# Kernel optimization log

Hardware: AMD Instinct MI355X
Metric: run time of the kernel (lower is better)

Reference implementation:

```python
import jax, jax.numpy as jnp
import numpy as np

N_NODES = 100000
N_EDGES = 1600000
EMBED = 64
HEADS = 8
HEAD_DIM = EMBED // HEADS
FFN = 4 * EMBED
EPS = 1e-5


def _layer_norm(x, g, b):
    m = jnp.mean(x, axis=-1, keepdims=True)
    v = jnp.mean(jnp.square(x - m), axis=-1, keepdims=True)
    return (x - m) * jax.lax.rsqrt(v + EPS) * g + b


def setup_inputs() -> dict:
    key = jax.random.key(0)
    ks = jax.random.split(key, 10)
    s = lambda fan_in: 1.0 / np.sqrt(fan_in)
    x = jax.random.normal(ks[0], (N_NODES, EMBED), dtype=jnp.float32)
    edge_indices = jax.random.randint(ks[1], (2, N_EDGES), 0, N_NODES, dtype=jnp.int64)
    attn_w = jax.random.uniform(ks[2], (EMBED, 3 * EMBED), jnp.float32, -s(EMBED), s(EMBED))
    attn_b = jnp.zeros((3 * EMBED,), jnp.float32)
    w1 = jax.random.uniform(ks[3], (EMBED, FFN), jnp.float32, -s(EMBED), s(EMBED))
    b1 = jnp.zeros((FFN,), jnp.float32)
    w2 = jax.random.uniform(ks[4], (FFN, EMBED), jnp.float32, -s(FFN), s(FFN))
    b2 = jnp.zeros((EMBED,), jnp.float32)
    ln1_g = jnp.ones((EMBED,), jnp.float32)
    ln1_b = jnp.zeros((EMBED,), jnp.float32)
    ln2_g = jnp.ones((EMBED,), jnp.float32)
    ln2_b = jnp.zeros((EMBED,), jnp.float32)
    return {"x": x, "edge_indices": edge_indices, "attn_w": attn_w, "attn_b": attn_b,
            "w1": w1, "b1": b1, "w2": w2, "b2": b2,
            "ln1_g": ln1_g, "ln1_b": ln1_b, "ln2_g": ln2_g, "ln2_b": ln2_b}


def _self_attention(x, edge_indices, attn_w, attn_b):
    n = x.shape[0]
    row, col = edge_indices[0], edge_indices[1]
    scale = EMBED ** (-0.5)  # note: original scales by embed_dim**-0.5
    qkv = (x @ attn_w + attn_b).reshape(n, HEADS, 3 * HEAD_DIM)
    q, k, v = jnp.split(qkv, 3, axis=2)  # each [N, H, Dh]
    alpha = jnp.sum(q[row] * k[col], axis=2) * scale  # [E, H]
    # sparse per-row softmax via segment reductions
    m = jax.ops.segment_max(alpha, row, num_segments=n)  # [N, H]
    e = jnp.exp(alpha - m[row])
    denom = jax.ops.segment_sum(e, row, num_segments=n)  # [N, H]
    weights = e / denom[row]  # [E, H]
    vals = v[col] * weights[:, :, None]  # [E, H, Dh]
    out = jax.ops.segment_sum(vals, row, num_segments=n)  # [N, H, Dh]
    return out.reshape(n, EMBED)


def reference(x, edge_indices, attn_w, attn_b, w1, b1, w2, b2, ln1_g, ln1_b, ln2_g, ln2_b):
    # post-norm (norm_first=False), dropout=0
    x = _layer_norm(x + _self_attention(x, edge_indices, attn_w, attn_b), ln1_g, ln1_b)
    ffn = jax.nn.relu(x @ w1 + b1) @ w2 + b2
    x = _layer_norm(x + ffn, ln2_g, ln2_b)
    return x
```

## Files before the change

kernel.cpp:

```cpp
#include <hip/hip_runtime.h>
#include <hip/hip_bf16.h>
#include <hip/hip_fp8.h>


#define WAVE 64
constexpr int BUCKET_SHIFT = 7;
constexpr int NBMAX = 800;

typedef __attribute__((ext_vector_type(8))) short bf16x8;
typedef __attribute__((ext_vector_type(4))) float f32x4;
typedef __attribute__((ext_vector_type(2))) float f32x2;

union BF8 {
  bf16x8 v;
  unsigned u[4];
};

__device__ __forceinline__ float bfbits_lo(unsigned u) {
  return __uint_as_float(u << 16);
}
__device__ __forceinline__ float bfbits_hi(unsigned u) {
  return __uint_as_float(u & 0xffff0000u);
}
__device__ __forceinline__ unsigned f2bf_pk(float a, float b) {
  unsigned ua = __float_as_uint(a);
  unsigned ub = __float_as_uint(b);
  ua = (ua + 0x7fff + ((ua >> 16) & 1)) >> 16;
  ub = (ub + 0x7fff + ((ub >> 16) & 1)) & 0xffff0000u;
  return ua | ub;
}
__device__ __forceinline__ unsigned short f2bf1(float a) {
  unsigned ua = __float_as_uint(a);
  ua = (ua + 0x7fff + ((ua >> 16) & 1)) >> 16;
  return (unsigned short)ua;
}

#if defined(__has_builtin)
#if __has_builtin(__builtin_amdgcn_cvt_pk_f32_fp8) && \
    __has_builtin(__builtin_amdgcn_cvt_pk_fp8_f32)
#define FP8_HW 1
#endif
#endif

#ifdef FP8_HW
#define FP8PK0(w) __builtin_amdgcn_cvt_pk_f32_fp8((int)(w), false)
#define FP8PK1(w) __builtin_amdgcn_cvt_pk_f32_fp8((int)(w), true)
__device__ __forceinline__ unsigned fp8enc4(float a, float b, float c,
                                            float d) {
  int r = __builtin_amdgcn_cvt_pk_fp8_f32(a, b, 0, false);
  r = __builtin_amdgcn_cvt_pk_fp8_f32(c, d, r, true);
  return (unsigned)r;
}
#else
__device__ __forceinline__ f32x2 fp8pk_sw(unsigned w, int sh) {
  __hip_fp8_e4m3 a, b;
  a.__x = (unsigned char)((w >> sh) & 0xff);
  b.__x = (unsigned char)((w >> (sh + 8)) & 0xff);
  f32x2 r;
  r.x = (float)a;
  r.y = (float)b;
  return r;
}
#define FP8PK0(w) fp8pk_sw((w), 0)
#define FP8PK1(w) fp8pk_sw((w), 16)
__device__ __forceinline__ unsigned fp8enc4(float a, float b, float c,
                                            float d) {
  __hip_fp8_e4m3 qa(a), qb(b), qc(c), qd(d);
  return (unsigned)qa.__x | ((unsigned)qb.__x << 8) |
         ((unsigned)qc.__x << 16) | ((unsigned)qd.__x << 24);
}
#endif

__device__ __forceinline__ float dot8_fp8(uint2 w, const float qv[8]) {
  f32x2 a = FP8PK0(w.x), b = FP8PK1(w.x), c = FP8PK0(w.y), d = FP8PK1(w.y);
  return a.x * qv[0] + a.y * qv[1] + b.x * qv[2] + b.y * qv[3] + c.x * qv[4] +
         c.y * qv[5] + d.x * qv[6] + d.y * qv[7];
}
__device__ __forceinline__ void acc8_fp8(uint2 w, float ee, float acc[8]) {
  f32x2 a = FP8PK0(w.x), b = FP8PK1(w.x), c = FP8PK0(w.y), d = FP8PK1(w.y);
  acc[0] += ee * a.x;
  acc[1] += ee * a.y;
  acc[2] += ee * b.x;
  acc[3] += ee * b.y;
  acc[4] += ee * c.x;
  acc[5] += ee * c.y;
  acc[6] += ee * d.x;
  acc[7] += ee * d.y;
}

__device__ __forceinline__ bool detect_is64_block(const int* __restrict__ e,
                                                  int* sflag) {
  if (threadIdx.x == 0) *sflag = 0;
  __syncthreads();
  unsigned v = 0;
  for (int i = threadIdx.x; i < 2048; i += blockDim.x)
    v |= (unsigned)e[2 * i + 1];
  if (v) atomicOr(sflag, 1);
  __syncthreads();
  return *sflag == 0;
}

__device__ __forceinline__ int edge_row(const int* e, int i, bool is64) {
  return is64 ? e[2 * (size_t)i] : e[i];
}
__device__ __forceinline__ int edge_col(const int* e, int i, int E, bool is64) {
  return is64 ? e[2 * ((size_t)E + i)] : e[(size_t)E + i];
}

__global__ __launch_bounds__(256) void cvt_w2(
    const float* __restrict__ aw, const float* __restrict__ w1,
    const float* __restrict__ w2, unsigned short* __restrict__ awT,
    unsigned short* __restrict__ w1T, unsigned short* __restrict__ w2T) {
  int tid = blockIdx.x * 256 + threadIdx.x;
  int stride = gridDim.x * 256;
  for (int i = tid; i < 192 * 64; i += stride) {
    int nn = i >> 6, kk = i & 63;
    awT[i] = f2bf1(aw[kk * 192 + nn]);
  }
  for (int i = tid; i < 256 * 64; i += stride) {
    int nn = i >> 6, kk = i & 63;
    w1T[i] = f2bf1(w1[kk * 256 + nn]);
  }
  for (int i = tid; i < 64 * 256; i += stride) {
    int nn = i >> 8, kk = i & 255;
    w2T[i] = f2bf1(w2[kk * 64 + nn]);
  }
}

__global__ __launch_bounds__(256) void bucket_count(const int* __restrict__ e,
                                                    int E,
                                                    int* __restrict__ tot,
                                                    int NB, int CH) {
  __shared__ int h[NBMAX];
  __shared__ int sflag;
  bool is64 = detect_is64_block(e, &sflag);
  for (int b = threadIdx.x; b < NB; b += 256) h[b] = 0;
  __syncthreads();
  int c0 = blockIdx.x * CH, c1 = min(E, c0 + CH);
  for (int i = c0 + threadIdx.x; i < c1; i += 256)
    atomicAdd(&h[edge_row(e, i, is64) >> BUCKET_SHIFT], 1);
  __syncthreads();
  for (int b = threadIdx.x; b < NB; b += 256)
    if (h[b]) atomicAdd(&tot[b], h[b]);
}

__global__ __launch_bounds__(1024) void scan_buckets(
    const int* __restrict__ tot, int NB, int* __restrict__ bucketstart,
    int* __restrict__ cursor) {
  __shared__ int wtot[16], wexcl[16];
  int tid = threadIdx.x;
  int lane = tid & 63, wid = tid >> 6;
  int v = (tid < NB) ? tot[tid] : 0;
  int incl = v;
#pragma unroll
  for (int m = 1; m < WAVE; m <<= 1) {
    int t = __shfl_up(incl, m);
    if (lane >= m) incl += t;
  }
  if (lane == 63) wtot[wid] = incl;
  __syncthreads();
  if (tid < 16) {
    int w = wtot[tid];
    int wi = w;
#pragma unroll
    for (int m = 1; m < 16; m <<= 1) {
      int t = __shfl_up(wi, m);
      if (tid >= m) wi += t;
    }
    wexcl[tid] = wi - w;
  }
  __syncthreads();
  int excl = wexcl[wid] + incl - v;
  if (tid < NB) {
    bucketstart[tid] = excl;
    cursor[tid] = excl;
  }
  if (tid == NB - 1) bucketstart[NB] = excl + v;
}

__global__ __launch_bounds__(256) void bucket_place(const int* __restrict__ e,
                                                    int E,
                                                    int* __restrict__ cursor,
                                                    unsigned* __restrict__ ebuf,
                                                    int NB, int CH) {
  __shared__ int cnt[NBMAX];
  __shared__ int sflag;
  bool is64 = detect_is64_block(e, &sflag);
  for (int b = threadIdx.x; b < NB; b += 256) cnt[b] = 0;
  __syncthreads();
  int c0 = blockIdx.x * CH, c1 = min(E, c0 + CH);
  for (int i = c0 + threadIdx.x; i < c1; i += 256)
    atomicAdd(&cnt[edge_row(e, i, is64) >> BUCKET_SHIFT], 1);
  __syncthreads();
  for (int b = threadIdx.x; b < NB; b += 256) {
    int c = cnt[b];
    cnt[b] = c ? atomicAdd(&cursor[b], c) : 0;
  }
  __syncthreads();
  for (int i = c0 + threadIdx.x; i < c1; i += 256) {
    int r = edge_row(e, i, is64);
    int c = edge_col(e, i, E, is64);
    int pos = atomicAdd(&cnt[r >> BUCKET_SHIFT], 1);
    ebuf[pos] = ((unsigned)(r & 127) << 17) | (unsigned)c;
  }
}

__global__ __launch_bounds__(256) void bucket_csr(
    const unsigned* __restrict__ ebuf, const int* __restrict__ bucketstart,
    int* __restrict__ ecol, int* __restrict__ rowstart, int n, int NB, int E) {
  __shared__ int cnt[128], offs[128], cur[128];
  const int b = blockIdx.x;
  const int tid = threadIdx.x;
  const int start = bucketstart[b];
  const int end = bucketstart[b + 1];
  if (tid < 128) cnt[tid] = 0;
  __syncthreads();
  for (int i = start + tid; i < end; i += 256)
    atomicAdd(&cnt[(ebuf[i] >> 17) & 127], 1);
  __syncthreads();
  if (tid < 128) offs[tid] = cnt[tid];
  __syncthreads();
  for (int s = 1; s < 128; s <<= 1) {
    int t = 0;
    if (tid < 128 && tid >= s) t = offs[tid - s];
    __syncthreads();
    if (tid < 128) offs[tid] += t;
    __syncthreads();
  }
  if (tid < 128) {
    int excl = offs[tid] - cnt[tid];
    cur[tid] = start + excl;
    int gr = (b << BUCKET_SHIFT) + tid;
    if (gr < n) rowstart[gr] = start + excl;
  }
  if (b == NB - 1 && tid == 0) rowstart[n] = E;
  __syncthreads();
  for (int i = start + tid; i < end; i += 256) {
    unsigned p = ebuf[i];
    int pos = atomicAdd(&cur[(p >> 17) & 127], 1);
    ecol[pos] = (int)(p & 0x1FFFF);
  }
}

template <int NCOLS, int K, int MODE, bool AFP32>
__global__ __launch_bounds__(256) void mfma_gemm(
    const void* __restrict__ A, const unsigned short* __restrict__ BT,
    const float* __restrict__ bias, unsigned short* __restrict__ out_q,
    unsigned char* __restrict__ out_kv8, unsigned short* __restrict__ out_h,
    const unsigned short* __restrict__ resid, const float* __restrict__ g,
    const float* __restrict__ beta, float* __restrict__ out_f, int n) {
  constexpr int KP = K + 8;
  constexpr int NT = NCOLS / 16;
  constexpr int NKC = K / 32;
  __shared__ unsigned short sB[NCOLS * KP];

  const int tid = threadIdx.x;
  {
    const uint4* src = (const uint4*)BT;
    for (int idx = tid; idx < NCOLS * K / 8; idx += 256) {
      int nn = idx / (K / 8), kq = idx % (K / 8);
      *(uint4*)&sB[nn * KP + kq * 8] = src[idx];
    }
  }
  __syncthreads();

  const int wid = tid >> 6, lane = tid & 63;
  const int l15 = lane & 15, quad = lane >> 4;
  const int rowbase = blockIdx.x * 128 + wid * 32;

  bf16x8 afrag[2][NKC];
#pragma unroll
  for (int rg = 0; rg < 2; rg++) {
    int row = rowbase + rg * 16 + l15;
    if (row >= n) row = n - 1;
    if (AFP32) {
      const float* Af = ((const float*)A) + (size_t)row * K;
#pragma unroll
      for (int kc = 0; kc < NKC; kc++) {
        float4 u0 = *(const float4*)(Af + kc * 32 + quad * 8);
        float4 u1 = *(const float4*)(Af + kc * 32 + quad * 8 + 4);
        BF8 t;
        t.u[0] = f2bf_pk(u0.x, u0.y);
        t.u[1] = f2bf_pk(u0.z, u0.w);
        t.u[2] = f2bf_pk(u1.x, u1.y);
        t.u[3] = f2bf_pk(u1.z, u1.w);
        afrag[rg][kc] = t.v;
      }
    } else {
      const bf16x8* ap = (const bf16x8*)((const unsigned short*)A + (size_t)row * K);
#pragma unroll
      for (int kc = 0; kc < NKC; kc++) afrag[rg][kc] = ap[kc * 4 + quad];
    }
  }

  f32x4 acc[2][NT];
#pragma unroll
  for (int rg = 0; rg < 2; rg++)
#pragma unroll
    for (int t = 0; t < NT; t++) acc[rg][t] = (f32x4){0.f, 0.f, 0.f, 0.f};

#pragma unroll
  for (int t = 0; t < NT; t++) {
#pragma unroll
    for (int kc = 0; kc < NKC; kc++) {
      bf16x8 b = *(const bf16x8*)&sB[(t * 16 + l15) * KP + kc * 32 + quad * 8];
      acc[0][t] = __builtin_amdgcn_mfma_f32_16x16x32_bf16(b, afrag[0][kc],
                                                          acc[0][t], 0, 0, 0);
      acc[1][t] = __builtin_amdgcn_mfma_f32_16x16x32_bf16(b, afrag[1][kc],
                                                          acc[1][t], 0, 0, 0);
    }
  }

  if (MODE == 0) {
#pragma unroll
    for (int rg = 0; rg < 2; rg++) {
      int row = rowbase + rg * 16 + l15;
      if (row >= n) continue;
#pragma unroll
      for (int t = 0; t < NT; t++) {
        int c0 = t * 16 + quad * 4;
        float4 bb = *(const float4*)&bias[c0];
        float v0 = acc[rg][t].x + bb.x, v1 = acc[rg][t].y + bb.y;
        float v2 = acc[rg][t].z + bb.z, v3 = acc[rg][t].w + bb.w;
        int hh = c0 / 24, rem = c0 % 24;
        if (rem < 8) {
          v0 *= 0.125f;
          v1 *= 0.125f;
          v2 *= 0.125f;
          v3 *= 0.125f;
          *(uint2*)(out_q + (size_t)row * 64 + hh * 8 + rem) =
              make_uint2(f2bf_pk(v0, v1), f2bf_pk(v2, v3));
        } else if (rem < 16) {
          *(unsigned*)(out_kv8 + (size_t)row * 128 + hh * 8 + (rem - 8)) =
              fp8enc4(v0, v1, v2, v3);
        } else {
          *(unsigned*)(out_kv8 + (size_t)row * 128 + 64 + hh * 8 + (rem - 16)) =
              fp8enc4(v0, v1, v2, v3);
        }
      }
    }
  } else if (MODE == 1) {
#pragma unroll
    for (int rg = 0; rg < 2; rg++) {
      int row = rowbase + rg * 16 + l15;
      if (row >= n) continue;
#pragma unroll
      for (int t = 0; t < NT; t++) {
        int c0 = t * 16 + quad * 4;
        float4 bb = *(const float4*)&bias[c0];
        float v0 = fmaxf(acc[rg][t].x + bb.x, 0.f);
        float v1 = fmaxf(acc[rg][t].y + bb.y, 0.f);
        float v2 = fmaxf(acc[rg][t].z + bb.z, 0.f);
        float v3 = fmaxf(acc[rg][t].w + bb.w, 0.f);
        *(uint2*)(out_h + (size_t)row * NCOLS + c0) =
            make_uint2(f2bf_pk(v0, v1), f2bf_pk(v2, v3));
      }
    }
  } else {
#pragma unroll
    for (int rg = 0; rg < 2; rg++) {
      int row = rowbase + rg * 16 + l15;
      bool ok = row < n;
      int rowc = ok ? row : n - 1;
      float vals[4][4];
      float ps = 0.f, pq = 0.f;
#pragma unroll
      for (int t = 0; t < 4; t++) {
        int c0 = t * 16 + quad * 4;
        float4 bb = *(const float4*)&bias[c0];
        uint2 rr = *(const uint2*)&resid[(size_t)rowc * 64 + c0];
        vals[t][0] = acc[rg][t].x + bb.x + bfbits_lo(rr.x);
        vals[t][1] = acc[rg][t].y + bb.y + bfbits_hi(rr.x);
        vals[t][2] = acc[rg][t].z + bb.z + bfbits_lo(rr.y);
        vals[t][3] = acc[rg][t].w + bb.w + bfbits_hi(rr.y);
#pragma unroll
        for (int r = 0; r < 4; r++) {
          ps += vals[t][r];
          pq += vals[t][r] * vals[t][r];
        }
      }
      ps += __shfl_xor(ps, 16);
      ps += __shfl_xor(ps, 32);
      pq += __shfl_xor(pq, 16);
      pq += __shfl_xor(pq, 32);
      float mean = ps * (1.f / 64.f);
      float var = pq * (1.f / 64.f) - mean * mean;
      float inv = rsqrtf(var + 1e-5f);
      if (ok) {
#pragma unroll
        for (int t = 0; t < 4; t++) {
          int c0 = t * 16 + quad * 4;
          float4 gg = *(const float4*)&g[c0];
          float4 be = *(const float4*)&beta[c0];
          float4 o = make_float4((vals[t][0] - mean) * inv * gg.x + be.x,
                                 (vals[t][1] - mean) * inv * gg.y + be.y,
                                 (vals[t][2] - mean) * inv * gg.z + be.z,
                                 (vals[t][3] - mean) * inv * gg.w + be.w);
          *(float4*)&out_f[(size_t)row * 64 + c0] = o;
        }
      }
    }
  }
}

__global__ __launch_bounds__(256) void attn_ln_kernel(
    const float* __restrict__ x, const unsigned short* __restrict__ qbuf,
    const unsigned char* __restrict__ kv8, const int* __restrict__ rowstart,
    const int* __restrict__ ecol, const float* __restrict__ g,
    const float* __restrict__ beta, unsigned short* __restrict__ x1b, int n) {
  int wave = threadIdx.x >> 6;
  int lane = threadIdx.x & 63;
  int node = blockIdx.x * 4 + wave;
  if (node >= n) return;
  const int e = lane >> 3, h = lane & 7;

  uint4 qp = ((const uint4*)(qbuf + (size_t)node * 64))[h];
  float qv[8] = {bfbits_lo(qp.x), bfbits_hi(qp.x), bfbits_lo(qp.y),
                 bfbits_hi(qp.y), bfbits_lo(qp.z), bfbits_hi(qp.z),
                 bfbits_lo(qp.w), bfbits_hi(qp.w)};

  int start = rowstart[node];
  int cnt = rowstart[node + 1] - start;
  float den = 0.f;
  float acc[8] = {0.f, 0.f, 0.f, 0.f, 0.f, 0.f, 0.f, 0.f};

  int iters = (cnt + 7) >> 3;
  int it = 0;
  for (; it + 2 <= iters; it += 2) {
    int i0 = it * 8 + e;
    int i1 = i0 + 8;
    bool v1 = i1 < cnt;
    int c0 = ecol[start + i0];
    int c1 = ecol[start + (v1 ? i1 : i0)];
    const unsigned char* r0 = kv8 + (size_t)c0 * 128 + h * 8;
    const unsigned char* r1 = kv8 + (size_t)c1 * 128 + h * 8;
    uint2 kw0 = *(const uint2*)r0;
    uint2 vw0 = *(const uint2*)(r0 + 64);
    uint2 kw1 = *(const uint2*)r1;
    uint2 vw1 = *(const uint2*)(r1 + 64);
    float a0 = dot8_fp8(kw0, qv);
    float a1 = dot8_fp8(kw1, qv);
    float e0 = __expf(a0);
    float e1 = v1 ? __expf(a1) : 0.f;
    den += e0 + e1;
    acc8_fp8(vw0, e0, acc);
    acc8_fp8(vw1, e1, acc);
  }
  if (it < iters) {
    int i0 = it * 8 + e;
    bool v0 = i0 < cnt;
    int c0 = ecol[start + (v0 ? i0 : 0)];
    const unsigned char* r0 = kv8 + (size_t)c0 * 128 + h * 8;
    uint2 kw0 = *(const uint2*)r0;
    uint2 vw0 = *(const uint2*)(r0 + 64);
    float a0 = dot8_fp8(kw0, qv);
    float e0 = v0 ? __expf(a0) : 0.f;
    den += e0;
    acc8_fp8(vw0, e0, acc);
  }

#pragma unroll
  for (int m = 8; m < 64; m <<= 1) {
    den += __shfl_xor(den, m);
#pragma unroll
    for (int j = 0; j < 8; j++) acc[j] += __shfl_xor(acc[j], m);
  }

  float invden = (cnt > 0) ? 1.f / den : 0.f;

  const float4* xr = (const float4*)(x + (size_t)node * 64 + h * 8);
  float4 xa = xr[0], xb4 = xr[1];
  float v[8];
  v[0] = xa.x + acc[0] * invden;
  v[1] = xa.y + acc[1] * invden;
  v[2] = xa.z + acc[2] * invden;
  v[3] = xa.w + acc[3] * invden;
  v[4] = xb4.x + acc[4] * invden;
  v[5] = xb4.y + acc[5] * invden;
  v[6] = xb4.z + acc[6] * invden;
  v[7] = xb4.w + acc[7] * invden;

  float ps = 0.f;
#pragma unroll
  for (int j = 0; j < 8; j++) ps += v[j];
#pragma unroll
  for (int m = 1; m < 8; m <<= 1) ps += __shfl_xor(ps, m);
  float mean = ps * (1.f / 64.f);
  float pq = 0.f;
#pragma unroll
  for (int j = 0; j < 8; j++) {
    float d = v[j] - mean;
    pq += d * d;
  }
#pragma unroll
  for (int m = 1; m < 8; m <<= 1) pq += __shfl_xor(pq, m);
  float inv = rsqrtf(pq * (1.f / 64.f) + 1e-5f);

  if (e == 0) {
    const float4* gr = (const float4*)(g + h * 8);
    const float4* br = (const float4*)(beta + h * 8);
    float4 ga = gr[0], gb = gr[1];
    float4 ba = br[0], bb = br[1];
    float o[8];
    o[0] = (v[0] - mean) * inv * ga.x + ba.x;
    o[1] = (v[1] - mean) * inv * ga.y + ba.y;
    o[2] = (v[2] - mean) * inv * ga.z + ba.z;
    o[3] = (v[3] - mean) * inv * ga.w + ba.w;
    o[4] = (v[4] - mean) * inv * gb.x + bb.x;
    o[5] = (v[5] - mean) * inv * gb.y + bb.y;
    o[6] = (v[6] - mean) * inv * gb.z + bb.z;
    o[7] = (v[7] - mean) * inv * gb.w + bb.w;
    *(uint4*)(x1b + (size_t)node * 64 + h * 8) =
        make_uint4(f2bf_pk(o[0], o[1]), f2bf_pk(o[2], o[3]),
                   f2bf_pk(o[4], o[5]), f2bf_pk(o[6], o[7]));
  }
}

extern "C" void kernel_launch(void* const* d_in, const int* in_sizes, int n_in,
                              void* d_out, int out_size, void* d_ws,
                              size_t ws_size, hipStream_t stream) {
  const float* x = (const float*)d_in[0];
  const int* edges = (const int*)d_in[1];
  const float* attn_w = (const float*)d_in[2];
  const float* attn_b = (const float*)d_in[3];
  const float* w1 = (const float*)d_in[4];
  const float* b1 = (const float*)d_in[5];
  const float* w2 = (const float*)d_in[6];
  const float* b2 = (const float*)d_in[7];
  const float* g1 = (const float*)d_in[8];
  const float* bb1 = (const float*)d_in[9];
  const float* g2 = (const float*)d_in[10];
  const float* bb2 = (const float*)d_in[11];

  const int N = in_sizes[0] / 64;
  const int E = in_sizes[1] / 2;
  const int NB = (N + 127) >> BUCKET_SHIFT;
  const int CH = (E + 255) / 256;

  char* ws = (char*)d_ws;
  size_t oq = 0;
  size_t okv = oq + (size_t)N * 128;
  size_t ox1b = okv + (size_t)N * 128;
  size_t oh = ox1b + (size_t)N * 128;
  size_t oawT = oh + (size_t)N * 512;
  size_t ow1T = oawT + 192 * 64 * 2;
  size_t ow2T = ow1T + 256 * 64 * 2;
  size_t oebuf = ow2T + 64 * 256 * 2;
  size_t oecol = oebuf + (size_t)E * 4;
  size_t orowstart = oecol + (size_t)E * 4;
  size_t otot = orowstart + (size_t)(N + 4) * 4;
  size_t obstart = otot + (size_t)(NBMAX) * 4;
  size_t ocursor = obstart + (size_t)(NBMAX + 4) * 4;

  unsigned short* qbuf = (unsigned short*)(ws + oq);
  unsigned char* kv8 = (unsigned char*)(ws + okv);
  unsigned short* x1b = (unsigned short*)(ws + ox1b);
  unsigned short* hbuf = (unsigned short*)(ws + oh);
  unsigned short* awT = (unsigned short*)(ws + oawT);
  unsigned short* w1T = (unsigned short*)(ws + ow1T);
  unsigned short* w2T = (unsigned short*)(ws + ow2T);
  unsigned* ebuf = (unsigned*)(ws + oebuf);
  int* ecol = (int*)(ws + oecol);
  int* rowstart = (int*)(ws + orowstart);
  int* tot = (int*)(ws + otot);
  int* bucketstart = (int*)(ws + obstart);
  int* cursor = (int*)(ws + ocursor);

  hipMemsetAsync(tot, 0, (size_t)NB * 4, stream);

  cvt_w2<<<32, 256, 0, stream>>>(attn_w, w1, w2, awT, w1T, w2T);

  bucket_count<<<256, 256, 0, stream>>>(edges, E, tot, NB, CH);
  scan_buckets<<<1, 1024, 0, stream>>>(tot, NB, bucketstart, cursor);
  bucket_place<<<256, 256, 0, stream>>>(edges, E, cursor, ebuf, NB, CH);
  bucket_csr<<<NB, 256, 0, stream>>>(ebuf, bucketstart, ecol, rowstart, N, NB,
                                     E);

  const int gblocks = (N + 127) / 128;

  mfma_gemm<192, 64, 0, true><<<gblocks, 256, 0, stream>>>(
      x, awT, attn_b, qbuf, kv8, nullptr, nullptr, nullptr, nullptr, nullptr,
      N);

  attn_ln_kernel<<<(N + 3) / 4, 256, 0, stream>>>(x, qbuf, kv8, rowstart, ecol,
                                                  g1, bb1, x1b, N);

  mfma_gemm<256, 64, 1, false><<<gblocks, 256, 0, stream>>>(
      x1b, w1T, b1, nullptr, nullptr, hbuf, nullptr, nullptr, nullptr, nullptr,
      N);

  mfma_gemm<64, 256, 2, false><<<gblocks, 256, 0, stream>>>(
      hbuf, w2T, b2, nullptr, nullptr, nullptr, x1b, g2, bb2, (float*)d_out,
      N);
}
```

Baseline: 284.0 us.

## Fuse FFN GEMMs through shared memory and read bf16 residual in attention

Merges the two FFN GEMMs into one kernel that keeps the 256-wide hidden activation in per-wave shared memory, so the N×256 bf16 hidden buffer no longer makes a round trip through global memory. The QKV GEMM now reads weights straight from global/L2 instead of staging them in LDS, and also writes a bf16 copy of x that the attention kernel reads in place of the fp32 x. The memset is folded into the weight-conversion kernel. The trade-offs are higher LDS use in the fused FFN, which may lower occupancy, weight fragments fetched from global memory, and a bf16-rounded residual in the first layer norm.

```diff
diff --git a/kernel.cpp b/kernel.cpp
--- a/kernel.cpp
+++ b/kernel.cpp
@@ -14,6 +14,7 @@
 union BF8 {
   bf16x8 v;
   unsigned u[4];
+  uint4 q;
 };
 
 __device__ __forceinline__ float bfbits_lo(unsigned u) {
@@ -110,9 +111,11 @@
 __global__ __launch_bounds__(256) void cvt_w2(
     const float* __restrict__ aw, const float* __restrict__ w1,
     const float* __restrict__ w2, unsigned short* __restrict__ awT,
-    unsigned short* __restrict__ w1T, unsigned short* __restrict__ w2T) {
+    unsigned short* __restrict__ w1T, unsigned short* __restrict__ w2T,
+    int* __restrict__ tot, int NB) {
   int tid = blockIdx.x * 256 + threadIdx.x;
   int stride = gridDim.x * 256;
+  for (int i = tid; i < NB; i += stride) tot[i] = 0;
   for (int i = tid; i < 192 * 64; i += stride) {
     int nn = i >> 6, kk = i & 63;
     awT[i] = f2bf1(aw[kk * 192 + nn]);
@@ -242,68 +245,49 @@
   }
 }
 
-template <int NCOLS, int K, int MODE, bool AFP32>
-__global__ __launch_bounds__(256) void mfma_gemm(
-    const void* __restrict__ A, const unsigned short* __restrict__ BT,
-    const float* __restrict__ bias, unsigned short* __restrict__ out_q,
-    unsigned char* __restrict__ out_kv8, unsigned short* __restrict__ out_h,
-    const unsigned short* __restrict__ resid, const float* __restrict__ g,
-    const float* __restrict__ beta, float* __restrict__ out_f, int n) {
-  constexpr int KP = K + 8;
-  constexpr int NT = NCOLS / 16;
-  constexpr int NKC = K / 32;
-  __shared__ unsigned short sB[NCOLS * KP];
-
+__global__ __launch_bounds__(256) void qkv_gemm(
+    const float* __restrict__ x, const unsigned short* __restrict__ awT,
+    const float* __restrict__ bias, unsigned short* __restrict__ qbuf,
+    unsigned char* __restrict__ kv8, unsigned short* __restrict__ xb, int n) {
   const int tid = threadIdx.x;
-  {
-    const uint4* src = (const uint4*)BT;
-    for (int idx = tid; idx < NCOLS * K / 8; idx += 256) {
-      int nn = idx / (K / 8), kq = idx % (K / 8);
-      *(uint4*)&sB[nn * KP + kq * 8] = src[idx];
-    }
-  }
-  __syncthreads();
-
   const int wid = tid >> 6, lane = tid & 63;
   const int l15 = lane & 15, quad = lane >> 4;
   const int rowbase = blockIdx.x * 128 + wid * 32;
 
-  bf16x8 afrag[2][NKC];
+  bf16x8 afrag[2][2];
 #pragma unroll
   for (int rg = 0; rg < 2; rg++) {
     int row = rowbase + rg * 16 + l15;
-    if (row >= n) row = n - 1;
-    if (AFP32) {
-      const float* Af = ((const float*)A) + (size_t)row * K;
-#pragma unroll
-      for (int kc = 0; kc < NKC; kc++) {
-        float4 u0 = *(const float4*)(Af + kc * 32 + quad * 8);
-        float4 u1 = *(const float4*)(Af + kc * 32 + quad * 8 + 4);
-        BF8 t;
-        t.u[0] = f2bf_pk(u0.x, u0.y);
-        t.u[1] = f2bf_pk(u0.z, u0.w);
-        t.u[2] = f2bf_pk(u1.x, u1.y);
-        t.u[3] = f2bf_pk(u1.z, u1.w);
-        afrag[rg][kc] = t.v;
-      }
-    } else {
-      const bf16x8* ap = (const bf16x8*)((const unsigned short*)A + (size_t)row * K);
-#pragma unroll
-      for (int kc = 0; kc < NKC; kc++) afrag[rg][kc] = ap[kc * 4 + quad];
-    }
-  }
-
-  f32x4 acc[2][NT];
+    int rowc = (row < n) ? row : n - 1;
+    const float* Af = x + (size_t)rowc * 64;
+#pragma unroll
+    for (int kc = 0; kc < 2; kc++) {
+      float4 u0 = *(const float4*)(Af + kc * 32 + quad * 8);
+      float4 u1 = *(const float4*)(Af + kc * 32 + quad * 8 + 4);
+      BF8 t;
+      t.u[0] = f2bf_pk(u0.x, u0.y);
+      t.u[1] = f2bf_pk(u0.z, u0.w);
+      t.u[2] = f2bf_pk(u1.x, u1.y);
+      t.u[3] = f2bf_pk(u1.z, u1.w);
+      afrag[rg][kc] = t.v;
+      if (row < n)
+        *(uint4*)(xb + (size_t)row * 64 + kc * 32 + quad * 8) = t.q;
+    }
+  }
+
+  f32x4 acc[2][12];
 #pragma unroll
   for (int rg = 0; rg < 2; rg++)
 #pragma unroll
-    for (int t = 0; t < NT; t++) acc[rg][t] = (f32x4){0.f, 0.f, 0.f, 0.f};
-
-#pragma unroll
-  for (int t = 0; t < NT; t++) {
-#pragma unroll
-    for (int kc = 0; kc < NKC; kc++) {
-      bf16x8 b = *(const bf16x8*)&sB[(t * 16 + l15) * KP + kc * 32 + quad * 8];
+    for (int t = 0; t < 12; t++) acc[rg][t] = (f32x4){0.f, 0.f, 0.f, 0.f};
+
+#pragma unroll
+  for (int t = 0; t < 12; t++) {
+#pragma unroll
+    for (int kc = 0; kc < 2; kc++) {
+      bf16x8 b =
+          *(const bf16x8*)(awT + (size_t)(t * 16 + l15) * 64 + kc * 32 +
+                           quad * 8);
       acc[0][t] = __builtin_amdgcn_mfma_f32_16x16x32_bf16(b, afrag[0][kc],
                                                           acc[0][t], 0, 0, 0);
       acc[1][t] = __builtin_amdgcn_mfma_f32_16x16x32_bf16(b, afrag[1][kc],
@@ -311,100 +295,171 @@
     }
   }
 
-  if (MODE == 0) {
+#pragma unroll
+  for (int rg = 0; rg < 2; rg++) {
+    int row = rowbase + rg * 16 + l15;
+    if (row >= n) continue;
+#pragma unroll
+    for (int t = 0; t < 12; t++) {
+      int c0 = t * 16 + quad * 4;
+      float4 bb = *(const float4*)&bias[c0];
+      float v0 = acc[rg][t].x + bb.x, v1 = acc[rg][t].y + bb.y;
+      float v2 = acc[rg][t].z + bb.z, v3 = acc[rg][t].w + bb.w;
+      int hh = c0 / 24, rem = c0 % 24;
+      if (rem < 8) {
+        v0 *= 0.125f;
+        v1 *= 0.125f;
+        v2 *= 0.125f;
+        v3 *= 0.125f;
+        *(uint2*)(qbuf + (size_t)row * 64 + hh * 8 + rem) =
+            make_uint2(f2bf_pk(v0, v1), f2bf_pk(v2, v3));
+      } else if (rem < 16) {
+        *(unsigned*)(kv8 + (size_t)row * 128 + hh * 8 + (rem - 8)) =
+            fp8enc4(v0, v1, v2, v3);
+      } else {
+        *(unsigned*)(kv8 + (size_t)row * 128 + 64 + hh * 8 + (rem - 16)) =
+            fp8enc4(v0, v1, v2, v3);
+      }
+    }
+  }
+}
+
+constexpr int HP = 264;
+
+__global__ __launch_bounds__(256) void ffn_fused(
+    const unsigned short* __restrict__ x1b,
+    const unsigned short* __restrict__ w1T,
+    const unsigned short* __restrict__ w2T, const float* __restrict__ b1,
+    const float* __restrict__ b2, const float* __restrict__ g,
+    const float* __restrict__ beta, float* __restrict__ out, int n) {
+  __shared__ unsigned short sH[4 * 32 * HP];
+  const int tid = threadIdx.x;
+  const int wid = tid >> 6, lane = tid & 63;
+  const int l15 = lane & 15, quad = lane >> 4;
+  const int rowbase = blockIdx.x * 128 + wid * 32;
+  unsigned short* hw = sH + wid * 32 * HP;
+
+  bf16x8 afrag[2][2];
+#pragma unroll
+  for (int rg = 0; rg < 2; rg++) {
+    int row = rowbase + rg * 16 + l15;
+    if (row >= n) row = n - 1;
+    const bf16x8* ap = (const bf16x8*)(x1b + (size_t)row * 64);
+#pragma unroll
+    for (int kc = 0; kc < 2; kc++) afrag[rg][kc] = ap[kc * 4 + quad];
+  }
+
+#pragma unroll
+  for (int tq = 0; tq < 4; tq++) {
+    f32x4 acc1[2][4];
+#pragma unroll
+    for (int rg = 0; rg < 2; rg++)
+#pragma unroll
+      for (int t = 0; t < 4; t++) acc1[rg][t] = (f32x4){0.f, 0.f, 0.f, 0.f};
+#pragma unroll
+    for (int t4 = 0; t4 < 4; t4++) {
+      int t = tq * 4 + t4;
+#pragma unroll
+      for (int kc = 0; kc < 2; kc++) {
+        bf16x8 b =
+            *(const bf16x8*)(w1T + (size_t)(t * 16 + l15) * 64 + kc * 32 +
+                             quad * 8);
+        acc1[0][t4] = __builtin_amdgcn_mfma_f32_16x16x32_bf16(
+            b, afrag[0][kc], acc1[0][t4], 0, 0, 0);
+        acc1[1][t4] = __builtin_amdgcn_mfma_f32_16x16x32_bf16(
+            b, afrag[1][kc], acc1[1][t4], 0, 0, 0);
+      }
+    }
 #pragma unroll
     for (int rg = 0; rg < 2; rg++) {
-      int row = rowbase + rg * 16 + l15;
-      if (row >= n) continue;
-#pragma unroll
-      for (int t = 0; t < NT; t++) {
-        int c0 = t * 16 + quad * 4;
-        float4 bb = *(const float4*)&bias[c0];
-        float v0 = acc[rg][t].x + bb.x, v1 = acc[rg][t].y + bb.y;
-        float v2 = acc[rg][t].z + bb.z, v3 = acc[rg][t].w + bb.w;
-        int hh = c0 / 24, rem = c0 % 24;
-        if (rem < 8) {
-          v0 *= 0.125f;
-          v1 *= 0.125f;
-          v2 *= 0.125f;
-          v3 *= 0.125f;
-          *(uint2*)(out_q + (size_t)row * 64 + hh * 8 + rem) =
-              make_uint2(f2bf_pk(v0, v1), f2bf_pk(v2, v3));
-        } else if (rem < 16) {
-          *(unsigned*)(out_kv8 + (size_t)row * 128 + hh * 8 + (rem - 8)) =
-              fp8enc4(v0, v1, v2, v3);
-        } else {
-          *(unsigned*)(out_kv8 + (size_t)row * 128 + 64 + hh * 8 + (rem - 16)) =
-              fp8enc4(v0, v1, v2, v3);
-        }
-      }
-    }
-  } else if (MODE == 1) {
-#pragma unroll
-    for (int rg = 0; rg < 2; rg++) {
-      int row = rowbase + rg * 16 + l15;
-      if (row >= n) continue;
-#pragma unroll
-      for (int t = 0; t < NT; t++) {
-        int c0 = t * 16 + quad * 4;
-        float4 bb = *(const float4*)&bias[c0];
-        float v0 = fmaxf(acc[rg][t].x + bb.x, 0.f);
-        float v1 = fmaxf(acc[rg][t].y + bb.y, 0.f);
-        float v2 = fmaxf(acc[rg][t].z + bb.z, 0.f);
-        float v3 = fmaxf(acc[rg][t].w + bb.w, 0.f);
-        *(uint2*)(out_h + (size_t)row * NCOLS + c0) =
+#pragma unroll
+      for (int t4 = 0; t4 < 4; t4++) {
+        int c0 = (tq * 4 + t4) * 16 + quad * 4;
+        float4 bb = *(const float4*)&b1[c0];
+        float v0 = fmaxf(acc1[rg][t4].x + bb.x, 0.f);
+        float v1 = fmaxf(acc1[rg][t4].y + bb.y, 0.f);
+        float v2 = fmaxf(acc1[rg][t4].z + bb.z, 0.f);
+        float v3 = fmaxf(acc1[rg][t4].w + bb.w, 0.f);
+        *(uint2*)&hw[(rg * 16 + l15) * HP + c0] =
             make_uint2(f2bf_pk(v0, v1), f2bf_pk(v2, v3));
       }
     }
-  } else {
-#pragma unroll
-    for (int rg = 0; rg < 2; rg++) {
-      int row = rowbase + rg * 16 + l15;
-      bool ok = row < n;
-      int rowc = ok ? row : n - 1;
-      float vals[4][4];
-      float ps = 0.f, pq = 0.f;
+  }
+  __syncthreads();
+
+  f32x4 acc2[2][4];
+#pragma unroll
+  for (int rg = 0; rg < 2; rg++)
+#pragma unroll
+    for (int t = 0; t < 4; t++) acc2[rg][t] = (f32x4){0.f, 0.f, 0.f, 0.f};
+
+#pragma unroll
+  for (int kc = 0; kc < 8; kc++) {
+    bf16x8 hf[2];
+#pragma unroll
+    for (int rg = 0; rg < 2; rg++)
+      hf[rg] =
+          *(const bf16x8*)&hw[(rg * 16 + l15) * HP + kc * 32 + quad * 8];
+#pragma unroll
+    for (int t = 0; t < 4; t++) {
+      bf16x8 b =
+          *(const bf16x8*)(w2T + (size_t)(t * 16 + l15) * 256 + kc * 32 +
+                           quad * 8);
+      acc2[0][t] = __builtin_amdgcn_mfma_f32_16x16x32_bf16(b, hf[0], acc2[0][t],
+                                                           0, 0, 0);
+      acc2[1][t] = __builtin_amdgcn_mfma_f32_16x16x32_bf16(b, hf[1], acc2[1][t],
+                                                           0, 0, 0);
+    }
+  }
+
+#pragma unroll
+  for (int rg = 0; rg < 2; rg++) {
+    int row = rowbase + rg * 16 + l15;
+    bool ok = row < n;
+    int rowc = ok ? row : n - 1;
+    float vals[4][4];
+    float ps = 0.f, pq = 0.f;
+#pragma unroll
+    for (int t = 0; t < 4; t++) {
+      int c0 = t * 16 + quad * 4;
+      float4 bb = *(const float4*)&b2[c0];
+      uint2 rr = *(const uint2*)&x1b[(size_t)rowc * 64 + c0];
+      vals[t][0] = acc2[rg][t].x + bb.x + bfbits_lo(rr.x);
+      vals[t][1] = acc2[rg][t].y + bb.y + bfbits_hi(rr.x);
+      vals[t][2] = acc2[rg][t].z + bb.z + bfbits_lo(rr.y);
+      vals[t][3] = acc2[rg][t].w + bb.w + bfbits_hi(rr.y);
+#pragma unroll
+      for (int r = 0; r < 4; r++) {
+        ps += vals[t][r];
+        pq += vals[t][r] * vals[t][r];
+      }
+    }
+    ps += __shfl_xor(ps, 16);
+    ps += __shfl_xor(ps, 32);
+    pq += __shfl_xor(pq, 16);
+    pq += __shfl_xor(pq, 32);
+    float mean = ps * (1.f / 64.f);
+    float var = pq * (1.f / 64.f) - mean * mean;
+    float inv = rsqrtf(var + 1e-5f);
+    if (ok) {
 #pragma unroll
       for (int t = 0; t < 4; t++) {
         int c0 = t * 16 + quad * 4;
-        float4 bb = *(const float4*)&bias[c0];
-        uint2 rr = *(const uint2*)&resid[(size_t)rowc * 64 + c0];
-        vals[t][0] = acc[rg][t].x + bb.x + bfbits_lo(rr.x);
-        vals[t][1] = acc[rg][t].y + bb.y + bfbits_hi(rr.x);
-        vals[t][2] = acc[rg][t].z + bb.z + bfbits_lo(rr.y);
-        vals[t][3] = acc[rg][t].w + bb.w + bfbits_hi(rr.y);
-#pragma unroll
-        for (int r = 0; r < 4; r++) {
-          ps += vals[t][r];
-          pq += vals[t][r] * vals[t][r];
-        }
+        float4 gg = *(const float4*)&g[c0];
+        float4 be = *(const float4*)&beta[c0];
+        float4 o = make_float4((vals[t][0] - mean) * inv * gg.x + be.x,
+                               (vals[t][1] - mean) * inv * gg.y + be.y,
+                               (vals[t][2] - mean) * inv * gg.z + be.z,
+                               (vals[t][3] - mean) * inv * gg.w + be.w);
+        *(float4*)&out[(size_t)row * 64 + c0] = o;
       }
-      ps += __shfl_xor(ps, 16);
-      ps += __shfl_xor(ps, 32);
-      pq += __shfl_xor(pq, 16);
-      pq += __shfl_xor(pq, 32);
-      float mean = ps * (1.f / 64.f);
-      float var = pq * (1.f / 64.f) - mean * mean;
-      float inv = rsqrtf(var + 1e-5f);
-      if (ok) {
-#pragma unroll
-        for (int t = 0; t < 4; t++) {
-          int c0 = t * 16 + quad * 4;
-          float4 gg = *(const float4*)&g[c0];
-          float4 be = *(const float4*)&beta[c0];
-          float4 o = make_float4((vals[t][0] - mean) * inv * gg.x + be.x,
-                                 (vals[t][1] - mean) * inv * gg.y + be.y,
-                                 (vals[t][2] - mean) * inv * gg.z + be.z,
-                                 (vals[t][3] - mean) * inv * gg.w + be.w);
-          *(float4*)&out_f[(size_t)row * 64 + c0] = o;
-        }
-      }
     }
   }
 }
 
 __global__ __launch_bounds__(256) void attn_ln_kernel(
-    const float* __restrict__ x, const unsigned short* __restrict__ qbuf,
+    const unsigned short* __restrict__ xb,
+    const unsigned short* __restrict__ qbuf,
     const unsigned char* __restrict__ kv8, const int* __restrict__ rowstart,
     const int* __restrict__ ecol, const float* __restrict__ g,
     const float* __restrict__ beta, unsigned short* __restrict__ x1b, int n) {
@@ -468,17 +523,16 @@
 
   float invden = (cnt > 0) ? 1.f / den : 0.f;
 
-  const float4* xr = (const float4*)(x + (size_t)node * 64 + h * 8);
-  float4 xa = xr[0], xb4 = xr[1];
+  uint4 xr = *(const uint4*)(xb + (size_t)node * 64 + h * 8);
   float v[8];
-  v[0] = xa.x + acc[0] * invden;
-  v[1] = xa.y + acc[1] * invden;
-  v[2] = xa.z + acc[2] * invden;
-  v[3] = xa.w + acc[3] * invden;
-  v[4] = xb4.x + acc[4] * invden;
-  v[5] = xb4.y + acc[5] * invden;
-  v[6] = xb4.z + acc[6] * invden;
-  v[7] = xb4.w + acc[7] * invden;
+  v[0] = bfbits_lo(xr.x) + acc[0] * invden;
+  v[1] = bfbits_hi(xr.x) + acc[1] * invden;
+  v[2] = bfbits_lo(xr.y) + acc[2] * invden;
+  v[3] = bfbits_hi(xr.y) + acc[3] * invden;
+  v[4] = bfbits_lo(xr.z) + acc[4] * invden;
+  v[5] = bfbits_hi(xr.z) + acc[5] * invden;
+  v[6] = bfbits_lo(xr.w) + acc[6] * invden;
+  v[7] = bfbits_hi(xr.w) + acc[7] * invden;
 
   float ps = 0.f;
 #pragma unroll
@@ -541,8 +595,8 @@
   size_t oq = 0;
   size_t okv = oq + (size_t)N * 128;
   size_t ox1b = okv + (size_t)N * 128;
-  size_t oh = ox1b + (size_t)N * 128;
-  size_t oawT = oh + (size_t)N * 512;
+  size_t oxb = ox1b + (size_t)N * 128;
+  size_t oawT = oxb + (size_t)N * 128;
   size_t ow1T = oawT + 192 * 64 * 2;
   size_t ow2T = ow1T + 256 * 64 * 2;
   size_t oebuf = ow2T + 64 * 256 * 2;
@@ -555,7 +609,7 @@
   unsigned short* qbuf = (unsigned short*)(ws + oq);
   unsigned char* kv8 = (unsigned char*)(ws + okv);
   unsigned short* x1b = (unsigned short*)(ws + ox1b);
-  unsigned short* hbuf = (unsigned short*)(ws + oh);
+  unsigned short* xb = (unsigned short*)(ws + oxb);
   unsigned short* awT = (unsigned short*)(ws + oawT);
   unsigned short* w1T = (unsigned short*)(ws + ow1T);
   unsigned short* w2T = (unsigned short*)(ws + ow2T);
@@ -566,9 +620,7 @@
   int* bucketstart = (int*)(ws + obstart);
   int* cursor = (int*)(ws + ocursor);
 
-  hipMemsetAsync(tot, 0, (size_t)NB * 4, stream);
-
-  cvt_w2<<<32, 256, 0, stream>>>(attn_w, w1, w2, awT, w1T, w2T);
+  cvt_w2<<<32, 256, 0, stream>>>(attn_w, w1, w2, awT, w1T, w2T, tot, NB);
 
   bucket_count<<<256, 256, 0, stream>>>(edges, E, tot, NB, CH);
   scan_buckets<<<1, 1024, 0, stream>>>(tot, NB, bucketstart, cursor);
@@ -578,18 +630,11 @@
 
   const int gblocks = (N + 127) / 128;
 
-  mfma_gemm<192, 64, 0, true><<<gblocks, 256, 0, stream>>>(
-      x, awT, attn_b, qbuf, kv8, nullptr, nullptr, nullptr, nullptr, nullptr,
-      N);
-
-  attn_ln_kernel<<<(N + 3) / 4, 256, 0, stream>>>(x, qbuf, kv8, rowstart, ecol,
-                                                  g1, bb1, x1b, N);
-
-  mfma_gemm<256, 64, 1, false><<<gblocks, 256, 0, stream>>>(
-      x1b, w1T, b1, nullptr, nullptr, hbuf, nullptr, nullptr, nullptr, nullptr,
-      N);
-
-  mfma_gemm<64, 256, 2, false><<<gblocks, 256, 0, stream>>>(
-      hbuf, w2T, b2, nullptr, nullptr, nullptr, x1b, g2, bb2, (float*)d_out,
-      N);
-}
+  qkv_gemm<<<gblocks, 256, 0, stream>>>(x, awT, attn_b, qbuf, kv8, xb, N);
+
+  attn_ln_kernel<<<(N + 3) / 4, 256, 0, stream>>>(xb, qbuf, kv8, rowstart,
+                                                  ecol, g1, bb1, x1b, N);
+
+  ffn_fused<<<gblocks, 256, 0, stream>>>(x1b, w1T, w2T, b1, b2, g2, bb2,
+                                         (float*)d_out, N);
+}
```

Measured after the change: 287.3 us. Within noise of the previous version (+1.2%).
